# Optimization experiments

Measured on AMD Instinct MI355X. Metric: run time of the kernel, lower is better.

Reference implementation:

```python
import jax, jax.numpy as jnp
import numpy as np

NUM_HEADS = 16


def setup_inputs() -> dict:
    key = jax.random.key(0)
    ks = jax.random.split(key, 4)
    B, C, T, D = 1, 1, 3072, 1024
    s = 1.0 / np.sqrt(D)
    return {
        "x": jax.random.normal(ks[0], (B, C, T, D), dtype=jnp.float32),
        "Wq": jax.random.normal(ks[1], (D, D), dtype=jnp.float32) * s,
        "bq": jnp.zeros((D,), dtype=jnp.float32),
        "Wk": jax.random.normal(ks[2], (D, D), dtype=jnp.float32) * s,
        "bk": jnp.zeros((D,), dtype=jnp.float32),
        "Wv": jax.random.normal(ks[3], (D, D), dtype=jnp.float32) * s,
        "bv": jnp.zeros((D,), dtype=jnp.float32),
        "gamma": jnp.float32(0.5),  # learned scalar; 0.0 at torch init, nonzero here for a meaningful signal
    }


def reference(x, Wq, bq, Wk, bk, Wv, bv, gamma):
    # x: (B, C, T, D); Linear acts on last dim (torch: y = x @ W.T + b)
    B, C, T, D = x.shape
    H = NUM_HEADS
    q = (jnp.einsum("bctd,ed->bcte", x, Wq) + bq).reshape(B, -1, T, H)  # (B, X, T, H), X = C*D/H
    k = (jnp.einsum("bctd,ed->bcte", x, Wk) + bk).reshape(B, -1, T, H)
    v = (jnp.einsum("bctd,ed->bcte", x, Wv) + bv).reshape(B, -1, T, H)
    q = q.transpose(0, 3, 2, 1)  # (B, H, T, X)
    k = k.transpose(0, 3, 1, 2)  # (B, H, X, T)
    energy = q @ k               # (B, H, T, T)  -- note: NO 1/sqrt(d) scaling, as in source
    attn = jax.nn.softmax(energy, axis=-1)
    v = v.transpose(0, 3, 2, 1)  # (B, H, T, X)
    out = attn @ v               # (B, H, T, X)
    out = out.transpose(0, 2, 3, 1).reshape(B, T, -1)  # (B, T, X*H) = (B, T, C*D)
    # residual broadcast: (B, T, C*D) + (B, C, T, D); valid since B == C == 1
    return gamma * out + x
```

## Files before the change

kernel.cpp:

```cpp
#include <hip/hip_runtime.h>


typedef _Float16 v8h __attribute__((ext_vector_type(8)));
typedef _Float16 v4h __attribute__((ext_vector_type(4)));
typedef __fp16   v2pk __attribute__((ext_vector_type(2)));
typedef __fp16   v4pk __attribute__((ext_vector_type(4)));
typedef float    v4f __attribute__((ext_vector_type(4)));

#define TSEQ 3072
#define DM   1024
#define NH   16
#define XD   64
#define LOG2E 1.44269504f

__device__ __forceinline__ void async_load16(const void* g, void* l) {
  __builtin_amdgcn_global_load_lds(
      (const __attribute__((address_space(1))) unsigned int*)g,
      (__attribute__((address_space(3))) unsigned int*)l,
      16, 0, 0);
}

__device__ __forceinline__ float fexp2(float x) {
  float r; asm("v_exp_f32 %0, %1" : "=v"(r) : "v"(x)); return r;
}
__device__ __forceinline__ float flog2(float x) {
  float r; asm("v_log_f32 %0, %1" : "=v"(r) : "v"(x)); return r;
}

extern "C" __global__ __launch_bounds__(256) void cvt_kernel(
    const float* __restrict__ x, const float* __restrict__ wq,
    const float* __restrict__ wk, const float* __restrict__ wv,
    _Float16* __restrict__ xb, _Float16* __restrict__ wb)
{
  const int NX4 = (TSEQ * DM) / 4;
  const int NT  = NX4 * 2;
  for (int i = blockIdx.x * blockDim.x + threadIdx.x; i < NT;
       i += gridDim.x * blockDim.x) {
    float4 v;
    _Float16* dst;
    if (i < NX4) {
      v = ((const float4*)x)[i];
      dst = xb + (size_t)i * 4;
    } else {
      const int j = i - NX4;
      const int n = j >> 8;
      if (n < 1024)      v = ((const float4*)wq)[j];
      else if (n < 2048) v = ((const float4*)wk)[j - 262144];
      else               v = ((const float4*)wv)[j - 524288];
      dst = wb + (size_t)j * 4;
    }
    v4h h;
    h[0] = (_Float16)v.x; h[1] = (_Float16)v.y;
    h[2] = (_Float16)v.z; h[3] = (_Float16)v.w;
    *(v4h*)dst = h;
  }
}

extern "C" __global__ __launch_bounds__(256) void qkv_gemm_kernel(
    const _Float16* __restrict__ xb, const _Float16* __restrict__ wb,
    const float* __restrict__ bq, const float* __restrict__ bk,
    const float* __restrict__ bv,
    _Float16* __restrict__ qlin, _Float16* __restrict__ klin,
    _Float16* __restrict__ vlin)
{
  __shared__ _Float16 As[128 * 32];
  __shared__ _Float16 Bs[128 * 32];
  const int tid = threadIdx.x;
  const int w = tid >> 6, l = tid & 63;
  const int li = l & 15, lg = l >> 4;
  const int wm = w >> 1, wn = w & 1;
  const int bid = blockIdx.x;
  const int swz = (bid & 7) * 72 + (bid >> 3);
  const int m0 = (swz / 24) * 128, n0 = (swz % 24) * 128;
  v4f acc[4][4] = {};
  const int srow = l >> 2;
  const int scol = (l & 3) * 8;
  for (int k0 = 0; k0 < DM; k0 += 32) {
#pragma unroll
    for (int c = 0; c < 2; ++c) {
      const int rbase = c * 64 + w * 16;
      async_load16(xb + (size_t)(m0 + rbase + srow) * DM + k0 + scol, &As[rbase * 32]);
      async_load16(wb + (size_t)(n0 + rbase + srow) * DM + k0 + scol, &Bs[rbase * 32]);
    }
    __syncthreads();
    v8h af[4], bf[4];
#pragma unroll
    for (int mi = 0; mi < 4; ++mi)
      af[mi] = *(const v8h*)&As[(wm * 64 + mi * 16 + li) * 32 + lg * 8];
#pragma unroll
    for (int ni = 0; ni < 4; ++ni)
      bf[ni] = *(const v8h*)&Bs[(wn * 64 + ni * 16 + li) * 32 + lg * 8];
#pragma unroll
    for (int mi = 0; mi < 4; ++mi)
#pragma unroll
      for (int ni = 0; ni < 4; ++ni)
        acc[mi][ni] = __builtin_amdgcn_mfma_f32_16x16x32_f16(
            af[mi], bf[ni], acc[mi][ni], 0, 0, 0);
    __syncthreads();
  }
  const int which = n0 >> 10;
  const int ebase = n0 & 1023;
  const float* bias = which == 0 ? bq : (which == 1 ? bk : bv);
  _Float16* outp = which == 0 ? qlin : (which == 1 ? klin : vlin);
#pragma unroll
  for (int mi = 0; mi < 4; ++mi)
#pragma unroll
    for (int r = 0; r < 4; ++r) {
      const int t = m0 + wm * 64 + mi * 16 + lg * 4 + r;
#pragma unroll
      for (int ni = 0; ni < 4; ++ni) {
        const int e = ebase + wn * 64 + ni * 16 + li;
        outp[(size_t)t * DM + e] = (_Float16)(acc[mi][ni][r] + bias[e]);
      }
    }
}

extern "C" __global__ __launch_bounds__(256) void repack_kernel(
    const _Float16* __restrict__ qlin, const _Float16* __restrict__ klin,
    const _Float16* __restrict__ vlin,
    _Float16* __restrict__ qh, _Float16* __restrict__ kh,
    _Float16* __restrict__ vt)
{
  const int NE = NH * TSEQ * XD;
  for (int g = blockIdx.x * blockDim.x + threadIdx.x; g < 3 * NE;
       g += gridDim.x * blockDim.x) {
    if (g < 2 * NE) {
      const int gg = (g < NE) ? g : g - NE;
      const int xx = gg & 63;
      const int rest = gg >> 6;
      const int h = rest / TSEQ;
      const int i = rest - h * TSEQ;
      const int t = xx * 48 + (i >> 6);
      const int e = ((i & 63) << 4) + h;
      if (g < NE) qh[gg] = qlin[t * DM + e];
      else        kh[gg] = (_Float16)((float)klin[t * DM + e] * LOG2E);
    } else {
      const int o = g - 2 * NE;
      const int j = o % TSEQ;
      const int rest = o / TSEQ;
      const int xx = rest & 63;
      const int h = rest >> 6;
      const int t = xx * 48 + (j >> 6);
      const int e = ((j & 63) << 4) + h;
      vt[o] = vlin[t * DM + e];
    }
  }
}

extern "C" __global__ __launch_bounds__(256, 2) void attn_kernel(
    const _Float16* __restrict__ qh, const _Float16* __restrict__ kh,
    const _Float16* __restrict__ vt,
    _Float16* __restrict__ oP0, _Float16* __restrict__ oP1,
    float* __restrict__ sml0, float* __restrict__ sml1)
{
  __shared__ _Float16 SH[8192];
  const int tid = threadIdx.x;
  const int w = tid >> 6, l = tid & 63;
  const int li = l & 15, lg = l >> 4;
  const int b = blockIdx.x;
  const int rest = b >> 3;
  const int head = (b & 7) + 8 * (rest & 1);
  const int qt = (rest >> 1) & 15;
  const int jh = rest >> 5;
  const int i0 = qt * 192;
  const size_t hb = (size_t)head * TSEQ * XD;
  _Float16* oPart = jh ? oP1 : oP0;
  float* smlp = jh ? sml1 : sml0;

  v8h qf[3][2];
#pragma unroll
  for (int ct = 0; ct < 3; ++ct) {
    const _Float16* qrow = qh + hb + (size_t)(i0 + w * 48 + ct * 16 + li) * XD;
    qf[ct][0] = *(const v8h*)(qrow + lg * 8);
    qf[ct][1] = *(const v8h*)(qrow + 32 + lg * 8);
  }
  float m2[3] = {24.0f * LOG2E, 24.0f * LOG2E, 24.0f * LOG2E};
  float l4[3] = {0.0f, 0.0f, 0.0f};
  v4f oacc[4][3] = {};
  const int r8 = l >> 3, c8 = l & 7;
  const int jbase = jh * 1536;

  for (int j0 = jbase; j0 < jbase + 1536; j0 += 64) {
#pragma unroll
    for (int s = 0; s < 2; ++s) {
      const int n = w * 2 + s;
      const int row = n * 8 + r8;
      async_load16(kh + hb + (size_t)(j0 + row) * XD + ((c8 ^ (row & 7)) * 8),
                   &SH[n * 512]);
      async_load16(vt + hb + (size_t)row * TSEQ + j0 + ((c8 ^ (row & 7)) * 8),
                   &SH[4096 + n * 512]);
    }
    __syncthreads();
    const _Float16* Kc = &SH[0];
    const _Float16* Vc = &SH[4096];

    v4f e4[3][4];
#pragma unroll
    for (int kt = 0; kt < 4; ++kt) {
      const int krow = kt * 16 + li;
      const v8h kf0 = *(const v8h*)&Kc[krow * 64 + ((lg ^ (li & 7)) * 8)];
      const v8h kf1 = *(const v8h*)&Kc[krow * 64 + (((4 + lg) ^ (li & 7)) * 8)];
#pragma unroll
      for (int ct = 0; ct < 3; ++ct) {
        v4f a = {-m2[ct], -m2[ct], -m2[ct], -m2[ct]};
        a = __builtin_amdgcn_mfma_f32_16x16x32_f16(kf0, qf[ct][0], a, 0, 0, 0);
        a = __builtin_amdgcn_mfma_f32_16x16x32_f16(kf1, qf[ct][1], a, 0, 0, 0);
        e4[ct][kt] = a;
      }
    }

    float gm = -1.0e30f;
#pragma unroll
    for (int ct = 0; ct < 3; ++ct)
#pragma unroll
      for (int kt = 0; kt < 4; ++kt)
        gm = fmaxf(fmaxf(gm, fmaxf(e4[ct][kt][0], e4[ct][kt][1])),
                   fmaxf(e4[ct][kt][2], e4[ct][kt][3]));
    if (__any(gm > 11.5f)) {
#pragma unroll
      for (int ct = 0; ct < 3; ++ct) {
        float rm = -1.0e30f;
#pragma unroll
        for (int kt = 0; kt < 4; ++kt)
          rm = fmaxf(fmaxf(rm, fmaxf(e4[ct][kt][0], e4[ct][kt][1])),
                     fmaxf(e4[ct][kt][2], e4[ct][kt][3]));
        rm = fmaxf(rm, __shfl_xor(rm, 16, 64));
        rm = fmaxf(rm, __shfl_xor(rm, 32, 64));
        rm = fmaxf(rm, 0.0f);
        const float fs = fexp2(-rm);
#pragma unroll
        for (int kt = 0; kt < 4; ++kt)
#pragma unroll
          for (int rr = 0; rr < 4; ++rr) e4[ct][kt][rr] -= rm;
        l4[ct] *= fs;
#pragma unroll
        for (int mi = 0; mi < 4; ++mi) oacc[mi][ct] *= fs;
        m2[ct] += rm;
      }
    }

    v4h pv[3][4];
#pragma unroll
    for (int ct = 0; ct < 3; ++ct) {
#pragma unroll
      for (int kt = 0; kt < 4; ++kt) {
        const float p0 = fexp2(e4[ct][kt][0]);
        const float p1 = fexp2(e4[ct][kt][1]);
        const float p2 = fexp2(e4[ct][kt][2]);
        const float p3 = fexp2(e4[ct][kt][3]);
        const v2pk lo = __builtin_amdgcn_cvt_pkrtz(p0, p1);
        const v2pk hi = __builtin_amdgcn_cvt_pkrtz(p2, p3);
        const v4pk pk = __builtin_shufflevector(lo, hi, 0, 1, 2, 3);
        pv[ct][kt] = __builtin_bit_cast(v4h, pk);
        l4[ct] += (p0 + p1) + (p2 + p3);
      }
    }

#pragma unroll
    for (int mi = 0; mi < 4; ++mi) {
      const int vrow = mi * 16 + li;
      const int vb = vrow * 64 + (lg & 1) * 4;
#pragma unroll
      for (int kt = 0; kt < 4; ++kt) {
        const v4h vf = *(const v4h*)&Vc[vb + (((kt * 2 + (lg >> 1)) ^ (li & 7)) * 8)];
#pragma unroll
        for (int ct = 0; ct < 3; ++ct)
          oacc[mi][ct] = __builtin_amdgcn_mfma_f32_16x16x16f16(
              vf, pv[ct][kt], oacc[mi][ct], 0, 0, 0);
      }
    }
    __syncthreads();
  }

#pragma unroll
  for (int ct = 0; ct < 3; ++ct) {
    float ls = l4[ct];
    ls += __shfl_xor(ls, 16, 64);
    ls += __shfl_xor(ls, 32, 64);
    const float inv = 1.0f / ls;
    const int rl = w * 48 + ct * 16 + li;
    if (lg == 0) smlp[(size_t)(i0 + rl) * NH + head] = m2[ct] + flog2(ls);
#pragma unroll
    for (int mi = 0; mi < 4; ++mi) {
      v4h o4;
#pragma unroll
      for (int rr = 0; rr < 4; ++rr) o4[rr] = (_Float16)(oacc[mi][ct][rr] * inv);
      *(v4h*)&oPart[(size_t)(i0 + rl) * DM + head * 64 + mi * 16 + lg * 4] = o4;
    }
  }
}

extern "C" __global__ __launch_bounds__(256) void epilogue_kernel(
    const _Float16* __restrict__ oP0, const _Float16* __restrict__ oP1,
    const float* __restrict__ sml0, const float* __restrict__ sml1,
    const float* __restrict__ xin, const float* __restrict__ gscal,
    float* __restrict__ outp)
{
  __shared__ float po[8 * 1024];
  const int tid = threadIdx.x;
  const size_t t0 = (size_t)blockIdx.x * 8;
  {
    const int tr = tid >> 5;
    const int c0 = (tid & 31) * 32;
    const int h = c0 >> 6;
    const size_t t = t0 + tr;
    const float s0 = sml0[t * NH + h], s1 = sml1[t * NH + h];
    const float M = fmaxf(s0, s1);
    float u0 = fexp2(s0 - M), u1 = fexp2(s1 - M);
    const float dn = 1.0f / (u0 + u1);
    u0 *= dn; u1 *= dn;
    const _Float16* p0 = oP0 + t * DM + c0;
    const _Float16* p1 = oP1 + t * DM + c0;
#pragma unroll
    for (int c = 0; c < 4; ++c) {
      const v8h a = *(const v8h*)(p0 + c * 8);
      const v8h bb = *(const v8h*)(p1 + c * 8);
#pragma unroll
      for (int e = 0; e < 8; ++e)
        po[tr * 1024 + c0 + c * 8 + e] = u0 * (float)a[e] + u1 * (float)bb[e];
    }
  }
  __syncthreads();
  const float g = gscal[0];
  const int tr = tid >> 5;
  const int d0 = (tid & 31) * 32;
  const size_t rb = (t0 + tr) * DM + d0;
#pragma unroll
  for (int c4 = 0; c4 < 8; ++c4) {
    const float4 xi = *(const float4*)&xin[rb + c4 * 4];
    float4 rr;
    rr.x = g * po[tr * 1024 + ((c4 * 4 + 0) & 15) * 64 + ((d0 + c4 * 4 + 0) >> 4)] + xi.x;
    rr.y = g * po[tr * 1024 + ((c4 * 4 + 1) & 15) * 64 + ((d0 + c4 * 4 + 1) >> 4)] + xi.y;
    rr.z = g * po[tr * 1024 + ((c4 * 4 + 2) & 15) * 64 + ((d0 + c4 * 4 + 2) >> 4)] + xi.z;
    rr.w = g * po[tr * 1024 + ((c4 * 4 + 3) & 15) * 64 + ((d0 + c4 * 4 + 3) >> 4)] + xi.w;
    *(float4*)&outp[rb + c4 * 4] = rr;
  }
}

extern "C" void kernel_launch(void* const* d_in, const int* in_sizes, int n_in,
                              void* d_out, int out_size, void* d_ws, size_t ws_size,
                              hipStream_t stream)
{
  const float* x  = (const float*)d_in[0];
  const float* Wq = (const float*)d_in[1];
  const float* bq = (const float*)d_in[2];
  const float* Wk = (const float*)d_in[3];
  const float* bk = (const float*)d_in[4];
  const float* Wv = (const float*)d_in[5];
  const float* bv = (const float*)d_in[6];
  const float* gm = (const float*)d_in[7];
  float* outp = (float*)d_out;
  char* ws = (char*)d_ws;
  const size_t SZH = (size_t)TSEQ * DM * sizeof(_Float16);
  _Float16* xb   = (_Float16*)(ws);
  _Float16* wb   = (_Float16*)(ws + SZH);
  _Float16* qlin = (_Float16*)(ws + 2 * SZH);
  _Float16* klin = (_Float16*)(ws + 3 * SZH);
  _Float16* vlin = (_Float16*)(ws + 4 * SZH);
  _Float16* qhp  = (_Float16*)(ws + 5 * SZH);
  _Float16* khp  = (_Float16*)(ws + 6 * SZH);
  _Float16* vtp  = (_Float16*)(ws + 7 * SZH);
  _Float16* oP0  = (_Float16*)(ws);
  _Float16* oP1  = (_Float16*)(ws + SZH);
  float*    sml0 = (float*)(ws + 3 * SZH);
  float*    sml1 = sml0 + (size_t)TSEQ * NH;

  cvt_kernel<<<dim3(1024), dim3(256), 0, stream>>>(x, Wq, Wk, Wv, xb, wb);
  qkv_gemm_kernel<<<dim3(576), dim3(256), 0, stream>>>(xb, wb, bq, bk, bv,
                                                       qlin, klin, vlin);
  repack_kernel<<<dim3(4096), dim3(256), 0, stream>>>(qlin, klin, vlin,
                                                      qhp, khp, vtp);
  attn_kernel<<<dim3(512), dim3(256), 0, stream>>>(qhp, khp, vtp,
                                                   oP0, oP1, sml0, sml1);
  epilogue_kernel<<<dim3(384), dim3(256), 0, stream>>>(oP0, oP1, sml0, sml1,
                                                       x, gm, outp);
  (void)in_sizes; (void)n_in; (void)out_size; (void)ws_size;
}
```

Before: 134.7 us.

## Split attention key range four ways and merge partials in epilogue

```diff
diff --git a/kernel.cpp b/kernel.cpp
--- a/kernel.cpp
+++ b/kernel.cpp
@@ -147,11 +147,10 @@
   }
 }
 
-extern "C" __global__ __launch_bounds__(256, 2) void attn_kernel(
+extern "C" __global__ __launch_bounds__(256, 4) void attn_kernel(
     const _Float16* __restrict__ qh, const _Float16* __restrict__ kh,
     const _Float16* __restrict__ vt,
-    _Float16* __restrict__ oP0, _Float16* __restrict__ oP1,
-    float* __restrict__ sml0, float* __restrict__ sml1)
+    _Float16* __restrict__ oPb, float* __restrict__ smlb)
 {
   __shared__ _Float16 SH[8192];
   const int tid = threadIdx.x;
@@ -161,11 +160,11 @@
   const int rest = b >> 3;
   const int head = (b & 7) + 8 * (rest & 1);
   const int qt = (rest >> 1) & 15;
-  const int jh = rest >> 5;
+  const int jq = rest >> 5;
   const int i0 = qt * 192;
   const size_t hb = (size_t)head * TSEQ * XD;
-  _Float16* oPart = jh ? oP1 : oP0;
-  float* smlp = jh ? sml1 : sml0;
+  _Float16* oPart = oPb + (size_t)jq * TSEQ * DM;
+  float* smlp = smlb + (size_t)jq * TSEQ * NH;
 
   v8h qf[3][2];
 #pragma unroll
@@ -178,9 +177,9 @@
   float l4[3] = {0.0f, 0.0f, 0.0f};
   v4f oacc[4][3] = {};
   const int r8 = l >> 3, c8 = l & 7;
-  const int jbase = jh * 1536;
-
-  for (int j0 = jbase; j0 < jbase + 1536; j0 += 64) {
+  const int jbase = jq * 768;
+
+  for (int j0 = jbase; j0 < jbase + 768; j0 += 64) {
 #pragma unroll
     for (int s = 0; s < 2; ++s) {
       const int n = w * 2 + s;
@@ -291,8 +290,7 @@
 }
 
 extern "C" __global__ __launch_bounds__(256) void epilogue_kernel(
-    const _Float16* __restrict__ oP0, const _Float16* __restrict__ oP1,
-    const float* __restrict__ sml0, const float* __restrict__ sml1,
+    const _Float16* __restrict__ oPb, const float* __restrict__ smlb,
     const float* __restrict__ xin, const float* __restrict__ gscal,
     float* __restrict__ outp)
 {
@@ -304,20 +302,29 @@
     const int c0 = (tid & 31) * 32;
     const int h = c0 >> 6;
     const size_t t = t0 + tr;
-    const float s0 = sml0[t * NH + h], s1 = sml1[t * NH + h];
-    const float M = fmaxf(s0, s1);
-    float u0 = fexp2(s0 - M), u1 = fexp2(s1 - M);
-    const float dn = 1.0f / (u0 + u1);
-    u0 *= dn; u1 *= dn;
-    const _Float16* p0 = oP0 + t * DM + c0;
-    const _Float16* p1 = oP1 + t * DM + c0;
+    float s[4], u[4];
+#pragma unroll
+    for (int q = 0; q < 4; ++q) s[q] = smlb[(size_t)q * TSEQ * NH + t * NH + h];
+    const float M = fmaxf(fmaxf(s[0], s[1]), fmaxf(s[2], s[3]));
+    float usum = 0.0f;
+#pragma unroll
+    for (int q = 0; q < 4; ++q) { u[q] = fexp2(s[q] - M); usum += u[q]; }
+    const float dn = 1.0f / usum;
+#pragma unroll
+    for (int q = 0; q < 4; ++q) u[q] *= dn;
 #pragma unroll
     for (int c = 0; c < 4; ++c) {
-      const v8h a = *(const v8h*)(p0 + c * 8);
-      const v8h bb = *(const v8h*)(p1 + c * 8);
-#pragma unroll
-      for (int e = 0; e < 8; ++e)
-        po[tr * 1024 + c0 + c * 8 + e] = u0 * (float)a[e] + u1 * (float)bb[e];
+      float acc[8] = {};
+#pragma unroll
+      for (int q = 0; q < 4; ++q) {
+        const v8h a = *(const v8h*)(oPb + (size_t)q * TSEQ * DM + t * DM + c0 + c * 8);
+#pragma unroll
+        for (int e = 0; e < 8; ++e) acc[e] += u[q] * (float)a[e];
+      }
+      float4 w0 = {acc[0], acc[1], acc[2], acc[3]};
+      float4 w1 = {acc[4], acc[5], acc[6], acc[7]};
+      *(float4*)&po[tr * 1024 + c0 + c * 8]     = w0;
+      *(float4*)&po[tr * 1024 + c0 + c * 8 + 4] = w1;
     }
   }
   __syncthreads();
@@ -360,19 +367,15 @@
   _Float16* qhp  = (_Float16*)(ws + 5 * SZH);
   _Float16* khp  = (_Float16*)(ws + 6 * SZH);
   _Float16* vtp  = (_Float16*)(ws + 7 * SZH);
-  _Float16* oP0  = (_Float16*)(ws);
-  _Float16* oP1  = (_Float16*)(ws + SZH);
-  float*    sml0 = (float*)(ws + 3 * SZH);
-  float*    sml1 = sml0 + (size_t)TSEQ * NH;
+  _Float16* oPb  = (_Float16*)(ws);
+  float*    smlb = (float*)(ws + 4 * SZH);
 
   cvt_kernel<<<dim3(1024), dim3(256), 0, stream>>>(x, Wq, Wk, Wv, xb, wb);
   qkv_gemm_kernel<<<dim3(576), dim3(256), 0, stream>>>(xb, wb, bq, bk, bv,
                                                        qlin, klin, vlin);
   repack_kernel<<<dim3(4096), dim3(256), 0, stream>>>(qlin, klin, vlin,
                                                       qhp, khp, vtp);
-  attn_kernel<<<dim3(512), dim3(256), 0, stream>>>(qhp, khp, vtp,
-                                                   oP0, oP1, sml0, sml1);
-  epilogue_kernel<<<dim3(384), dim3(256), 0, stream>>>(oP0, oP1, sml0, sml1,
-                                                       x, gm, outp);
+  attn_kernel<<<dim3(1024), dim3(256), 0, stream>>>(qhp, khp, vtp, oPb, smlb);
+  epilogue_kernel<<<dim3(384), dim3(256), 0, stream>>>(oPb, smlb, x, gm, outp);
   (void)in_sizes; (void)n_in; (void)out_size; (void)ws_size;
 }
```

New measurement: 222.9 us. 1.65x slower.
